# Kernel tuning notes

Hardware: AMD Instinct MI355X
Metric: run time of the kernel (lower is better)

The kernel has to match this reference:

```python
import jax, jax.numpy as jnp
import numpy as np

EPS = 1e-08


def setup_inputs() -> dict:
    key = jax.random.key(0)
    k1, k2, k3 = jax.random.split(key, 3)
    B_img, B_txt, D = 8192, 8192, 512
    img_feature = jax.random.normal(k1, (B_img, D), dtype=jnp.float32)
    text_feature = jax.random.normal(k2, (B_txt, D), dtype=jnp.float32)
    text_lens = jax.random.randint(k3, (B_txt,), 1, 40, dtype=jnp.int32)
    return {"img_feature": img_feature, "text_feature": text_feature, "text_lens": text_lens}


def reference(img_feature, text_feature, text_lens):
    # Pairwise cosine similarity: equivalent to the original expand+mul+sum,
    # expressed as a GEMM of the raw features followed by norm division.
    # w12[i,j] = <img_i, txt_j>; sim = w12 / max(|img_i|*|txt_j|, eps)
    w12 = jnp.einsum('id,jd->ij', img_feature, text_feature)  # [B_img, B_txt]
    w1 = jnp.linalg.norm(img_feature, axis=-1)                # [B_img]
    w2 = jnp.linalg.norm(text_feature, axis=-1)               # [B_txt]
    denom = jnp.maximum(w1[:, None] * w2[None, :], EPS)
    return w12 / denom
```

## Files before the change

kernel.cpp:

```cpp
#include <hip/hip_runtime.h>
#include <hip/hip_bf16.h>

#define M 8192
#define N 8192
#define K 512
#define BM 128
#define BN 128
#define BK 32
#define NT (K / BK)

typedef __attribute__((ext_vector_type(8))) short bf16x8;
typedef __attribute__((ext_vector_type(4))) float f32x4;
typedef __attribute__((ext_vector_type(8))) unsigned short us8;

__device__ inline void gload_lds16(const void* g, void* l) {
  __builtin_amdgcn_global_load_lds(
      (const __attribute__((address_space(1))) unsigned int*)g,
      (__attribute__((address_space(3))) unsigned int*)l, 16, 0, 0);
}

#define BARRIER()                          \
  do {                                     \
    asm volatile("" ::: "memory");         \
    __builtin_amdgcn_s_barrier();          \
    asm volatile("" ::: "memory");         \
  } while (0)

__global__ __launch_bounds__(256) void prep_kernel(const float* __restrict__ img,
                                                   const float* __restrict__ txt,
                                                   unsigned short* __restrict__ Abf,
                                                   unsigned short* __restrict__ Bbf,
                                                   float* __restrict__ w1,
                                                   float* __restrict__ w2) {
  const int half = blockIdx.x >> 11;
  const int lb = blockIdx.x & 2047;
  const float* in = half ? txt : img;
  unsigned short* outb = half ? Bbf : Abf;
  float* norms = half ? w2 : w1;

  const int gw = (lb * 256 + threadIdx.x) >> 6;
  const int lane = threadIdx.x & 63;
  const float4* rp4 = (const float4*)(in + (size_t)gw * K);
  float4 v0 = rp4[lane * 2];
  float4 v1 = rp4[lane * 2 + 1];
  float ss = v0.x * v0.x + v0.y * v0.y + v0.z * v0.z + v0.w * v0.w +
             v1.x * v1.x + v1.y * v1.y + v1.z * v1.z + v1.w * v1.w;
  float f[8] = {v0.x, v0.y, v0.z, v0.w, v1.x, v1.y, v1.z, v1.w};
  us8 o;
#pragma unroll
  for (int i = 0; i < 8; ++i) {
    __hip_bfloat16 b = __float2bfloat16(f[i]);
    o[i] = *(unsigned short*)&b;
  }
  *(us8*)(outb + (size_t)gw * K + lane * 8) = o;
#pragma unroll
  for (int off = 32; off > 0; off >>= 1) ss += __shfl_down(ss, off, 64);
  if (lane == 0) norms[gw] = 1.0f / fmaxf(sqrtf(ss), 1e-4f);
}

__global__ __launch_bounds__(256, 4) void gemm_kernel(const unsigned short* __restrict__ A,
                                                      const unsigned short* __restrict__ B,
                                                      const float* __restrict__ iw1,
                                                      const float* __restrict__ iw2,
                                                      float* __restrict__ C) {
  __shared__ __align__(128) unsigned short As[2][BM * BK];
  __shared__ __align__(128) unsigned short Bs[3][BN * BK];

  const int tid = threadIdx.x;
  const int wave = tid >> 6;
  const int lane = tid & 63;
  const int wr = wave >> 1;
  const int wc = wave & 1;
  const int fr = lane & 15;
  const int fq = lane >> 4;

  const int xcd = blockIdx.x & 7;
  const int idx = blockIdx.x >> 3;
  const int bRow = (idx >> 3) * BM;
  const int bCol = (xcd * 8 + (idx & 7)) * BN;

  const int srow = lane >> 2;
  const int scol = (((lane & 3) ^ ((srow >> 1) & 3)) * 8);

  auto stageA = [&](int buf, int kt) {
#pragma unroll
    for (int c = 0; c < 2; ++c)
      gload_lds16(A + (size_t)(bRow + c * 64 + wave * 16 + srow) * K + kt * BK + scol,
                  (char*)&As[buf][0] + (c * 64 + wave * 16) * 64);
  };
  auto stageB = [&](int buf, int kt) {
#pragma unroll
    for (int c = 0; c < 2; ++c)
      gload_lds16(B + (size_t)(bCol + c * 64 + wave * 16 + srow) * K + kt * BK + scol,
                  (char*)&Bs[buf][0] + (c * 64 + wave * 16) * 64);
  };
  auto ldA = [&](int buf, int r) -> bf16x8 {
    return *(const bf16x8*)((const char*)&As[buf][0] + r * 64 +
                            ((fq ^ ((r >> 1) & 3)) * 16));
  };
  auto ldB = [&](int buf, int r) -> bf16x8 {
    return *(const bf16x8*)((const char*)&Bs[buf][0] + r * 64 +
                            ((fq ^ ((r >> 1) & 3)) * 16));
  };

  f32x4 acc[4][4] = {};

  stageA(0, 0);
  stageB(0, 0);
  stageB(1, 1);
  asm volatile("s_waitcnt vmcnt(2)" ::: "memory");
  BARRIER();

#pragma unroll
  for (int t = 0; t < NT; ++t) {
    const int cur = t & 1, nxt = cur ^ 1;
    const int bc = t % 3, b2 = (t + 2) % 3;

    if (t + 1 < NT) stageA(nxt, t + 1);
    if (t + 2 < NT) stageB(b2, t + 2);

    bf16x8 a[4], b[4];
#pragma unroll
    for (int m = 0; m < 4; ++m) a[m] = ldA(cur, wr * 64 + m * 16 + fr);
#pragma unroll
    for (int n = 0; n < 4; ++n) b[n] = ldB(bc, wc * 64 + n * 16 + fr);

    __builtin_amdgcn_s_setprio(1);
#pragma unroll
    for (int m = 0; m < 4; ++m)
#pragma unroll
      for (int n = 0; n < 4; ++n)
        acc[m][n] = __builtin_amdgcn_mfma_f32_16x16x32_bf16(a[m], b[n], acc[m][n], 0, 0, 0);
    __builtin_amdgcn_s_setprio(0);

    if (t < NT - 2) {
      asm volatile("s_waitcnt vmcnt(2)" ::: "memory");
    } else if (t == NT - 2) {
      asm volatile("s_waitcnt vmcnt(0)" ::: "memory");
    }
    BARRIER();
  }

  float i1v[4][4], i2v[4];
#pragma unroll
  for (int m = 0; m < 4; ++m)
#pragma unroll
    for (int r = 0; r < 4; ++r) i1v[m][r] = iw1[bRow + wr * 64 + m * 16 + fq * 4 + r];
#pragma unroll
  for (int n = 0; n < 4; ++n) i2v[n] = iw2[bCol + wc * 64 + n * 16 + fr];

#pragma unroll
  for (int m = 0; m < 4; ++m) {
    const int row0 = bRow + wr * 64 + m * 16 + fq * 4;
#pragma unroll
    for (int n = 0; n < 4; ++n) {
      const int col = bCol + wc * 64 + n * 16 + fr;
      f32x4 v = acc[m][n];
#pragma unroll
      for (int r = 0; r < 4; ++r)
        C[(size_t)(row0 + r) * N + col] = v[r] * i1v[m][r] * i2v[n];
    }
  }
}

extern "C" void kernel_launch(void* const* d_in, const int* in_sizes, int n_in,
                              void* d_out, int out_size, void* d_ws, size_t ws_size,
                              hipStream_t stream) {
  (void)in_sizes; (void)n_in; (void)out_size; (void)ws_size;
  const float* img = (const float*)d_in[0];
  const float* txt = (const float*)d_in[1];
  float* out = (float*)d_out;

  unsigned short* Abf = (unsigned short*)d_ws;
  unsigned short* Bbf = Abf + (size_t)M * K;
  float* w1 = (float*)(Bbf + (size_t)N * K);
  float* w2 = w1 + M;

  prep_kernel<<<4096, 256, 0, stream>>>(img, txt, Abf, Bbf, w1, w2);
  gemm_kernel<<<(M / BM) * (N / BN), 256, 0, stream>>>(Abf, Bbf, w1, w2, out);
}
```

Before: 109.2 us.

## Compute two column tiles per block and overlap first tile's stores with second's K-loop

Each workgroup now computes two adjacent 128x128 output tiles that share the A row panel, running a 32-step continuous K pipeline. The first tile's epilogue stores are split into chunks interleaved into the second tile's main loop, with vmcnt waits adjusted to account for outstanding stores. The goal is to hide the large fp32 output write behind MFMA work and to avoid the pipeline refill between tiles. The cost is doubled accumulator registers, which drops the occupancy target from 4 to 2 waves per SIMD, and halves the grid size.

```diff
diff --git a/kernel.cpp b/kernel.cpp
--- a/kernel.cpp
+++ b/kernel.cpp
@@ -7,7 +7,6 @@
 #define BM 128
 #define BN 128
 #define BK 32
-#define NT (K / BK)
 
 typedef __attribute__((ext_vector_type(8))) short bf16x8;
 typedef __attribute__((ext_vector_type(4))) float f32x4;
@@ -18,6 +17,8 @@
       (const __attribute__((address_space(1))) unsigned int*)g,
       (__attribute__((address_space(3))) unsigned int*)l, 16, 0, 0);
 }
+
+#define MEMFENCE() asm volatile("" ::: "memory")
 
 #define BARRIER()                          \
   do {                                     \
@@ -58,7 +59,7 @@
   if (lane == 0) norms[gw] = 1.0f / fmaxf(sqrtf(ss), 1e-4f);
 }
 
-__global__ __launch_bounds__(256, 4) void gemm_kernel(const unsigned short* __restrict__ A,
+__global__ __launch_bounds__(256, 2) void gemm_kernel(const unsigned short* __restrict__ A,
                                                       const unsigned short* __restrict__ B,
                                                       const float* __restrict__ iw1,
                                                       const float* __restrict__ iw2,
@@ -76,89 +77,121 @@
 
   const int xcd = blockIdx.x & 7;
   const int idx = blockIdx.x >> 3;
-  const int bRow = (idx >> 3) * BM;
-  const int bCol = (xcd * 8 + (idx & 7)) * BN;
+  const int bRow = (idx >> 2) * BM;
+  const int col0 = (xcd * 8 + (idx & 3) * 2) * BN;
+  const int col1 = col0 + BN;
 
   const int srow = lane >> 2;
   const int scol = (((lane & 3) ^ ((srow >> 1) & 3)) * 8);
 
-  auto stageA = [&](int buf, int kt) {
+  auto stageA = [&](int buf, int sl) {
 #pragma unroll
     for (int c = 0; c < 2; ++c)
-      gload_lds16(A + (size_t)(bRow + c * 64 + wave * 16 + srow) * K + kt * BK + scol,
+      gload_lds16(A + (size_t)(bRow + c * 64 + wave * 16 + srow) * K + sl * BK + scol,
                   (char*)&As[buf][0] + (c * 64 + wave * 16) * 64);
   };
-  auto stageB = [&](int buf, int kt) {
+  auto stageB = [&](int buf, int bCol, int sl) {
 #pragma unroll
     for (int c = 0; c < 2; ++c)
-      gload_lds16(B + (size_t)(bCol + c * 64 + wave * 16 + srow) * K + kt * BK + scol,
+      gload_lds16(B + (size_t)(bCol + c * 64 + wave * 16 + srow) * K + sl * BK + scol,
                   (char*)&Bs[buf][0] + (c * 64 + wave * 16) * 64);
   };
   auto ldA = [&](int buf, int r) -> bf16x8 {
-    return *(const bf16x8*)((const char*)&As[buf][0] + r * 64 +
-                            ((fq ^ ((r >> 1) & 3)) * 16));
+    return *(const bf16x8*)((const char*)&As[buf][0] + r * 64 + ((fq ^ ((r >> 1) & 3)) * 16));
   };
   auto ldB = [&](int buf, int r) -> bf16x8 {
-    return *(const bf16x8*)((const char*)&Bs[buf][0] + r * 64 +
-                            ((fq ^ ((r >> 1) & 3)) * 16));
-  };
-
-  f32x4 acc[4][4] = {};
+    return *(const bf16x8*)((const char*)&Bs[buf][0] + r * 64 + ((fq ^ ((r >> 1) & 3)) * 16));
+  };
+
+  float i1v[4][4], i2v0[4], i2v1[4];
+#pragma unroll
+  for (int m = 0; m < 4; ++m)
+#pragma unroll
+    for (int r = 0; r < 4; ++r) i1v[m][r] = iw1[bRow + wr * 64 + m * 16 + fq * 4 + r];
+#pragma unroll
+  for (int n = 0; n < 4; ++n) {
+    i2v0[n] = iw2[col0 + wc * 64 + n * 16 + fr];
+    i2v1[n] = iw2[col1 + wc * 64 + n * 16 + fr];
+  }
+
+  f32x4 acc0[4][4] = {}, acc1[4][4] = {};
+
+  auto colOfStep = [&](int g) { return (g >> 4) ? col1 : col0; };
 
   stageA(0, 0);
-  stageB(0, 0);
-  stageB(1, 1);
+  stageB(0, col0, 0);
+  stageB(1, col0, 1);
   asm volatile("s_waitcnt vmcnt(2)" ::: "memory");
   BARRIER();
 
-#pragma unroll
-  for (int t = 0; t < NT; ++t) {
-    const int cur = t & 1, nxt = cur ^ 1;
-    const int bc = t % 3, b2 = (t + 2) % 3;
-
-    if (t + 1 < NT) stageA(nxt, t + 1);
-    if (t + 2 < NT) stageB(b2, t + 2);
-
-    bf16x8 a[4], b[4];
-#pragma unroll
-    for (int m = 0; m < 4; ++m) a[m] = ldA(cur, wr * 64 + m * 16 + fr);
-#pragma unroll
-    for (int n = 0; n < 4; ++n) b[n] = ldB(bc, wc * 64 + n * 16 + fr);
-
-    __builtin_amdgcn_s_setprio(1);
-#pragma unroll
-    for (int m = 0; m < 4; ++m)
-#pragma unroll
-      for (int n = 0; n < 4; ++n)
-        acc[m][n] = __builtin_amdgcn_mfma_f32_16x16x32_bf16(a[m], b[n], acc[m][n], 0, 0, 0);
-    __builtin_amdgcn_s_setprio(0);
-
-    if (t < NT - 2) {
-      asm volatile("s_waitcnt vmcnt(2)" ::: "memory");
-    } else if (t == NT - 2) {
-      asm volatile("s_waitcnt vmcnt(0)" ::: "memory");
+  auto drain_chunk = [&](int mi) {
+    const int row0 = bRow + wr * 64 + mi * 16 + fq * 4;
+#pragma unroll
+    for (int n = 0; n < 4; ++n) {
+      const int col = col0 + wc * 64 + n * 16 + fr;
+#pragma unroll
+      for (int r = 0; r < 4; ++r)
+        C[(size_t)(row0 + r) * N + col] = acc0[mi][n][r] * i1v[mi][r] * i2v0[n];
     }
-    BARRIER();
-  }
-
-  float i1v[4][4], i2v[4];
-#pragma unroll
-  for (int m = 0; m < 4; ++m)
-#pragma unroll
-    for (int r = 0; r < 4; ++r) i1v[m][r] = iw1[bRow + wr * 64 + m * 16 + fq * 4 + r];
-#pragma unroll
-  for (int n = 0; n < 4; ++n) i2v[n] = iw2[bCol + wc * 64 + n * 16 + fr];
-
-#pragma unroll
-  for (int m = 0; m < 4; ++m) {
-    const int row0 = bRow + wr * 64 + m * 16 + fq * 4;
+  };
+
+#define KSTEP(GG, ACC, DRAIN_MI, WAITN)                                          \
+  do {                                                                           \
+    const int cur = (GG) & 1, nxt = cur ^ 1;                                     \
+    stageA(nxt, ((GG) + 1) & 15);                                                \
+    {                                                                            \
+      const int g2 = ((GG) + 2 > 31) ? 31 : ((GG) + 2);       \
+      stageB(((GG) + 2) % 3, colOfStep(g2), g2 & 15);                            \
+    }                                                                            \
+    MEMFENCE();                                                                  \
+    if ((DRAIN_MI) >= 0) drain_chunk(DRAIN_MI);                                  \
+    bf16x8 a[4], b[4];                                                           \
+    _Pragma("unroll") for (int m = 0; m < 4; ++m)                                \
+        a[m] = ldA(cur, wr * 64 + m * 16 + fr);                                  \
+    const int bc = (GG) % 3;                                                     \
+    _Pragma("unroll") for (int n = 0; n < 4; ++n)                                \
+        b[n] = ldB(bc, wc * 64 + n * 16 + fr);                                   \
+    __builtin_amdgcn_s_setprio(1);                                               \
+    _Pragma("unroll") for (int m = 0; m < 4; ++m)                                \
+        _Pragma("unroll") for (int n = 0; n < 4; ++n)                            \
+            ACC[m][n] = __builtin_amdgcn_mfma_f32_16x16x32_bf16(                 \
+                a[m], b[n], ACC[m][n], 0, 0, 0);                                 \
+    __builtin_amdgcn_s_setprio(0);                                               \
+    asm volatile("s_waitcnt vmcnt(" #WAITN ")" ::: "memory");                    \
+    BARRIER();                                                                   \
+  } while (0)
+
+#pragma unroll
+  for (int s = 0; s < 16; ++s) KSTEP(s, acc0, -1, 2);
+
+  KSTEP(16, acc1, -1, 2);
+  KSTEP(17, acc1, 0, 18);
+  KSTEP(18, acc1, -1, 2);
+  KSTEP(19, acc1, -1, 2);
+  KSTEP(20, acc1, -1, 2);
+  KSTEP(21, acc1, 1, 18);
+  KSTEP(22, acc1, -1, 2);
+  KSTEP(23, acc1, -1, 2);
+  KSTEP(24, acc1, -1, 2);
+  KSTEP(25, acc1, 2, 18);
+  KSTEP(26, acc1, -1, 2);
+  KSTEP(27, acc1, -1, 2);
+  KSTEP(28, acc1, -1, 2);
+  KSTEP(29, acc1, 3, 18);
+  KSTEP(30, acc1, -1, 2);
+  KSTEP(31, acc1, -1, 2);
+#undef KSTEP
+
+  asm volatile("s_waitcnt vmcnt(0)" ::: "memory");
+#pragma unroll
+  for (int mi = 0; mi < 4; ++mi) {
+    const int row0 = bRow + wr * 64 + mi * 16 + fq * 4;
 #pragma unroll
     for (int n = 0; n < 4; ++n) {
-      const int col = bCol + wc * 64 + n * 16 + fr;
-      f32x4 v = acc[m][n];
+      const int col = col1 + wc * 64 + n * 16 + fr;
 #pragma unroll
       for (int r = 0; r < 4; ++r)
-        C[(size_t)(row0 + r) * N + col] = v[r] * i1v[m][r] * i2v[n];
+        C[(size_t)(row0 + r) * N + col] = acc1[mi][n][r] * i1v[mi][r] * i2v1[n];
     }
   }
 }
@@ -177,5 +210,5 @@
   float* w2 = w1 + M;
 
   prep_kernel<<<4096, 256, 0, stream>>>(img, txt, Abf, Bbf, w1, w2);
-  gemm_kernel<<<(M / BM) * (N / BN), 256, 0, stream>>>(Abf, Bbf, w1, w2, out);
-}
+  gemm_kernel<<<2048, 256, 0, stream>>>(Abf, Bbf, w1, w2, out);
+}
```

Measured after the change: 125.6 us. 15.0% more time.
